# Kernel tuning notes

Hardware: AMD Instinct MI355X
Metric: run time of the kernel (lower is better)

## Reference

```python
import jax, jax.numpy as jnp
import numpy as np

N = 131072          # number of items ranked in one soft_rank call
CAPACITY = 3.0      # self.capcity in the torch module


def _pav_kl(y, w):
    """KL isotonic regression (non-increasing fit) via Pool-Adjacent-Violators.
    Pooled block value = logsumexp(y_block) - logsumexp(w_block).
    Matches torchsort / fast-soft-sort isotonic_kl. Sequential O(N)."""
    n = y.shape[0]

    def push(i, st):
        ly, lw, val, start, ptr = st
        ly = ly.at[ptr].set(y[i])
        lw = lw.at[ptr].set(w[i])
        val = val.at[ptr].set(y[i] - w[i])
        start = start.at[ptr].set(i)
        ptr = ptr + 1

        def cond(s):
            _, _, v, _, p = s
            return (p >= 2) & (v[p - 2] <= v[p - 1])

        def merge(s):
            ly, lw, v, stt, p = s
            ny = jnp.logaddexp(ly[p - 2], ly[p - 1])
            nw = jnp.logaddexp(lw[p - 2], lw[p - 1])
            return (ly.at[p - 2].set(ny), lw.at[p - 2].set(nw),
                    v.at[p - 2].set(ny - nw), stt, p - 1)

        return jax.lax.while_loop(cond, merge, (ly, lw, val, start, ptr))

    z = jnp.zeros((n,), y.dtype)
    st0 = (z, z, z, jnp.full((n,), n, jnp.int32), jnp.int32(0))
    ly, lw, val, start, ptr = jax.lax.fori_loop(0, n, push, st0)
    # invalidate stale stack slots, then map each element to its block value
    start = jnp.where(jnp.arange(n) < ptr, start, n)
    blk = jnp.searchsorted(start, jnp.arange(n), side='right') - 1
    return val[blk]


@jax.custom_vjp
def isotonic_kl(y, w):
    return _pav_kl(y, w)


def _iso_fwd(y, w):
    sol = _pav_kl(y, w)
    return sol, (y, w, sol)


def _iso_bwd(res, g):
    y, w, sol = res
    n = y.shape[0]
    # blocks = maximal runs of constant solution (exact equality by construction)
    blk = jnp.cumsum(jnp.concatenate([jnp.array([True]), sol[1:] != sol[:-1]])) - 1
    gsum = jax.ops.segment_sum(g, blk, num_segments=n)

    def seg_softmax(v):
        m = jax.ops.segment_max(v, blk, num_segments=n)
        lse = jnp.log(jax.ops.segment_sum(jnp.exp(v - m[blk]), blk, num_segments=n)) + m
        return jnp.exp(v - lse[blk])

    return seg_softmax(y) * gsum[blk], -seg_softmax(w) * gsum[blk]


isotonic_kl.defvjp(_iso_fwd, _iso_bwd)


def soft_rank_kl(scores):
    """torchsort.soft_rank(scores[None], regularization='kl'), strength=1, ascending."""
    n = scores.shape[0]
    w_log = jnp.log(jnp.arange(n, 0, -1, dtype=scores.dtype))  # log([n, ..., 1])
    perm = jnp.argsort(-scores)          # descending, stable
    s = scores[perm]
    sol = isotonic_kl(s, w_log)
    inv = jnp.argsort(perm)
    return jnp.exp(s - sol)[inv]


def setup_inputs() -> dict:
    key = jax.random.key(0)
    k = jax.random.split(key, 5)
    x = jax.random.normal(k[0], (N, 1), jnp.float32)
    # torch Linear default init bounds: 1/sqrt(fan_in)
    w1 = jax.random.uniform(k[1], (1, 32), jnp.float32, -1.0, 1.0)
    b1 = jax.random.uniform(k[2], (32,), jnp.float32, -1.0, 1.0)
    lim2 = 1.0 / np.sqrt(32.0)
    w2 = jax.random.uniform(k[3], (32, 1), jnp.float32, -lim2, lim2)
    b2 = jax.random.uniform(k[4], (1,), jnp.float32, -lim2, lim2)
    return {"x": x, "w1": w1, "b1": b1, "w2": w2, "b2": b2}


def reference(x, w1, b1, w2, b2):
    h = jnp.maximum(x @ w1 + b1, 0.0)            # [N, 32]
    scores = (h @ w2 + b2).reshape(-1)           # [N]
    ranks = soft_rank_kl(scores)                 # [N]
    other = jax.lax.stop_gradient(ranks) % CAPACITY
    ranks = (ranks - other) / CAPACITY + 1.0
    return ranks.reshape(-1, 1)
```

## Files before the change

### kernel.cpp

```cpp
#include <hip/hip_runtime.h>
#include <stdint.h>

typedef unsigned int u32;
typedef unsigned long long u64;

#define N_ITEMS 131072
#define NB 131072
#define NSLICE 8
#define CHUNK 64
#define NCHUNKS 2048
#define SCAN_BLOCKS 512
#define FIXSCALE 268435456.0f
#define FIXMASK ((1ull << 46) - 1)


__device__ __forceinline__ float wsumf(int s, int e) {
  return 0.5f * (float)(e - s + 1) * (float)(2 * N_ITEMS - s - e);
}

__device__ __forceinline__ float key_to_score(u32 key) {
  u32 m = ~key;
  u32 u = (m & 0x80000000u) ? (m ^ 0x80000000u) : ~m;
  return __uint_as_float(u);
}

#define LOG2E 1.4426950408889634f
__device__ __forceinline__ float fexp(float x) { return exp2f(x * LOG2E); }

__device__ __forceinline__ u32 bucket_of(u32 key, u32 kmin, u32 kmax) {
  double scale = (double)NB / ((double)(kmax - kmin) + 1.0);
  u32 b = (u32)((double)(key - kmin) * scale);
  return b < NB ? b : (NB - 1);
}


__global__ void score_key_kernel(const float* __restrict__ x,
                                 const float* __restrict__ w1,
                                 const float* __restrict__ b1,
                                 const float* __restrict__ w2,
                                 const float* __restrict__ b2,
                                 u32* __restrict__ keyRaw,
                                 u32* __restrict__ pmin, u32* __restrict__ pmax,
                                 u64* __restrict__ hist8, u64* __restrict__ flags) {
  __shared__ u32 r0[256], r1[256];
  int t = threadIdx.x;
  int i = blockIdx.x * 256 + t;
#pragma unroll
  for (int k = 0; k < NSLICE; ++k) hist8[(size_t)k * NB + i] = 0ull;
  if (i < SCAN_BLOCKS) flags[i] = 0ull;
  float xv = x[i];
  float s = b2[0];
#pragma unroll
  for (int j = 0; j < 32; ++j) {
    float h = fmaf(xv, w1[j], b1[j]);
    h = fmaxf(h, 0.0f);
    s = fmaf(h, w2[j], s);
  }
  u32 u = __float_as_uint(s);
  u32 m = u ^ ((u & 0x80000000u) ? 0xFFFFFFFFu : 0x80000000u);
  u32 key = ~m;
  keyRaw[i] = key;
  r0[t] = key; r1[t] = key;
  __syncthreads();
  for (int off = 128; off > 0; off >>= 1) {
    if (t < off) { r0[t] = min(r0[t], r0[t + off]); r1[t] = max(r1[t], r1[t + off]); }
    __syncthreads();
  }
  if (t == 0) { pmin[blockIdx.x] = r0[0]; pmax[blockIdx.x] = r1[0]; }
}


__global__ void hist_kernel(const u32* __restrict__ keyRaw,
                            const u32* __restrict__ pmin, const u32* __restrict__ pmax,
                            u64* __restrict__ hist8, u32* __restrict__ mm) {
  __shared__ u32 s0[256], s1[256];
  int t = threadIdx.x;
  s0[t] = min(pmin[t], pmin[t + 256]);
  s1[t] = max(pmax[t], pmax[t + 256]);
  __syncthreads();
  for (int off = 128; off > 0; off >>= 1) {
    if (t < off) { s0[t] = min(s0[t], s0[t + off]); s1[t] = max(s1[t], s1[t + off]); }
    __syncthreads();
  }
  u32 kmin = s0[0], kmax = s1[0];
  if (blockIdx.x == 0 && t == 0) { mm[0] = kmin; mm[1] = kmax; }
  int i = blockIdx.x * 256 + t;
  u32 key = keyRaw[i];
  u32 g = bucket_of(key, kmin, kmax);
  float smax = key_to_score(kmin);
  float v = fexp(key_to_score(key) - smax);
  u64 fix = (u64)fmaxf(1.0f, fmaf(v, FIXSCALE, 0.5f));
  size_t slice = (size_t)(blockIdx.x & (NSLICE - 1)) * NB;
  atomicAdd(&hist8[slice + g], (1ull << 46) | fix);
}


__global__ __launch_bounds__(256) void scan_pav_kernel(const u64* __restrict__ hist8,
                                                       u64* __restrict__ flags,
                                                       u32* __restrict__ cdf,
                                                       u32* __restrict__ cstart,
                                                       float* __restrict__ SY,
                                                       int* __restrict__ ST,
                                                       int* __restrict__ cnt) {
  __shared__ u32 sh[256];
  __shared__ float seL[256];
  __shared__ u32 cdfL[257];
  __shared__ u32 exclu_s;
  __shared__ u32 stkST[64][4];
  __shared__ float stkSY[64][4];
  int t = threadIdx.x, b = blockIdx.x;
  int i = b * 256 + t;
  u64 acc = 0;
#pragma unroll
  for (int c = 0; c < NSLICE; ++c) acc += hist8[(size_t)c * NB + i];
  u32 v = (u32)(acc >> 46);
  seL[t] = (float)(acc & FIXMASK) * (1.0f / FIXSCALE);
  sh[t] = v;
  __syncthreads();
  for (int off = 1; off < 256; off <<= 1) {
    u32 x2 = (t >= off) ? sh[t - off] : 0u;
    __syncthreads();
    sh[t] += x2;
    __syncthreads();
  }
  if (t == 0) {
    u32 agg = sh[255];
    if (b == 0) {
      atomicExch(&flags[0], (2ull << 32) | (u64)agg);
      exclu_s = 0u;
    } else {
      atomicExch(&flags[b], (1ull << 32) | (u64)agg);
      u32 ex = 0; int j = b - 1;
      for (;;) {
        u64 f = atomicAdd(&flags[j], 0ull);
        u32 st = (u32)(f >> 32);
        if (st == 0u) continue;
        ex += (u32)f;
        if (st == 2u) break;
        --j;
      }
      atomicExch(&flags[b], (2ull << 32) | (u64)(ex + agg));
      exclu_s = ex;
    }
  }
  __syncthreads();
  u32 exclu = exclu_s;
  u32 e = sh[t] - v + exclu;
  cdfL[t] = e;
  if (t == 255) cdfL[256] = exclu + sh[255];
  cdf[i] = e;
  if ((t & 63) == 0) cstart[i >> 6] = e;
  if (i == 0) cstart[NCHUNKS] = N_ITEMS;
  __syncthreads();
  if (t < 4) {
    int c = b * 4 + t;
    int ptr = 0; bool have = false;
    float syT = 0.0f; int stT = 0;
    for (int k = 0; k < 64; ++k) {
      u32 cs = cdfL[t * 64 + k], ce = cdfL[t * 64 + k + 1];
      if (ce == cs) continue;
      float syC = seL[t * 64 + k];
      int stC = (int)cs, eC = (int)ce - 1;
      while (have) {
        float SWc = wsumf(stC, eC);
        float SWt = wsumf(stT, stC - 1);
        if (!(syT * SWc <= syC * SWt)) break;
        syC += syT; stC = stT;
        if (ptr == 0) { have = false; break; }
        --ptr;
        stT = (int)stkST[ptr][t]; syT = stkSY[ptr][t];
      }
      if (have) { stkST[ptr][t] = (u32)stT; stkSY[ptr][t] = syT; ++ptr; }
      stT = stC; syT = syC; have = true;
    }
    int slotBase = c * 64;
    for (int k2 = 0; k2 < ptr; ++k2) {
      ST[slotBase + k2] = (int)stkST[k2][t];
      SY[slotBase + k2] = stkSY[k2][t];
    }
    int n = ptr;
    if (have) { ST[slotBase + n] = stT; SY[slotBase + n] = syT; ++n; }
    cnt[c] = n;
  }
}


__global__ void merge_multi_kernel(float* __restrict__ SY, int* __restrict__ ST,
                                   int* __restrict__ cnt, const u32* __restrict__ cstart,
                                   int l0, int L) {
  __shared__ int lcnt[64];
  __shared__ int ca[32], cb[32], cM[32];
  int t = threadIdx.x;
  int G = 1 << L;
  int SC = 1 << l0;
  int baseC = blockIdx.x * G * SC;
  if (t < G) lcnt[t] = cnt[baseC + t * SC];
  __syncthreads();
  for (int j = 0; j < L; ++j) {
    int P = G >> (j + 1);
    if (t < P) {
      int p = t;
      int kL = p << (j + 1), kR = kL + (1 << j);
      int slotL = (baseC + kL * SC) * 64, slotR = (baseC + kR * SC) * 64;
      int nL = lcnt[kL], nR = lcnt[kR];
      int a = 0, b = 0, hasM = 0;
      if (nL > 0 && nR > 0) {
        int gstartR = (int)cstart[baseC + kR * SC];
        int gendR   = (int)cstart[baseC + (kR + (1 << j)) * SC];
        float SYL = SY[slotL + nL - 1]; int stL = ST[slotL + nL - 1];
        float SYR = SY[slotR];
        int eR = (nR > 1) ? (ST[slotR + 1] - 1) : (gendR - 1);
        float SWL = wsumf(stL, gstartR - 1);
        float SWR = wsumf(gstartR, eR);
        if (SYL * SWR <= SYR * SWL) {
          hasM = 1;
          float SYM = SYL + SYR; int Ms = stL, Me = eR;
          a = 1; b = 1;
          for (;;) {
            float SWM = wsumf(Ms, Me);
            if (a < nL) {
              float SYe = SY[slotL + nL - 1 - a]; int ste = ST[slotL + nL - 1 - a];
              float SWe = wsumf(ste, Ms - 1);
              if (SYe * SWM <= SYM * SWe) { SYM += SYe; Ms = ste; ++a; continue; }
            }
            if (b < nR) {
              float SYb = SY[slotR + b]; int sb = ST[slotR + b];
              int eb = (b + 1 < nR) ? (ST[slotR + b + 1] - 1) : (gendR - 1);
              float SWb = wsumf(sb, eb);
              if (SYM * SWb <= SYb * SWM) { SYM += SYb; Me = eb; ++b; continue; }
            }
            break;
          }
          SY[slotL + nL - a] = SYM; ST[slotL + nL - a] = Ms;
        }
      }
      ca[p] = a; cb[p] = b; cM[p] = hasM;
    }
    __syncthreads();
    for (int p = 0; p < P; ++p) {
      int kL = p << (j + 1), kR = kL + (1 << j);
      int nL = lcnt[kL], nR = lcnt[kR];
      int a = ca[p], b = cb[p], hasM = cM[p];
      int slotL = (baseC + kL * SC) * 64, slotR = (baseC + kR * SC) * 64;
      int destBase = slotL + nL - a + hasM;
      int srcBase = slotR + b;
      int ncopy = nR - b;
      for (int off = 0; off < ncopy; off += blockDim.x) {
        int k2 = off + t; bool act = k2 < ncopy;
        float vs = 0.f; int vt = 0;
        if (act) { vs = SY[srcBase + k2]; vt = ST[srcBase + k2]; }
        __syncthreads();
        if (act) { SY[destBase + k2] = vs; ST[destBase + k2] = vt; }
        __syncthreads();
      }
    }
    __syncthreads();
    if (t < P) {
      int p = t; int kL = p << (j + 1), kR = kL + (1 << j);
      lcnt[kL] = lcnt[kL] - ca[p] + cM[p] + (lcnt[kR] - cb[p]);
    }
    __syncthreads();
  }
  if (t == 0) cnt[baseC] = lcnt[0];
}


__global__ void out_kernel(const u32* __restrict__ keyRaw, const u32* __restrict__ mm,
                           const u32* __restrict__ cdf,
                           const float* __restrict__ SY, const int* __restrict__ ST,
                           const int* __restrict__ cnt, float* __restrict__ out) {
  int i = blockIdx.x * 256 + threadIdx.x;
  u32 key = keyRaw[i];
  u32 kmin = mm[0], kmax = mm[1];
  float smax = key_to_score(kmin);
  u32 g = bucket_of(key, kmin, kmax);
  int p = (int)cdf[g];
  int m = cnt[0];
  int lo = 0, hi = m - 1;
  while (lo < hi) {
    int mid = (lo + hi + 1) >> 1;
    if (ST[mid] <= p) lo = mid; else hi = mid - 1;
  }
  int s0 = ST[lo];
  int e0 = (lo + 1 < m) ? (ST[lo + 1] - 1) : (N_ITEMS - 1);
  float SW = wsumf(s0, e0);
  float s = key_to_score(key);
  float rank = fexp(s - smax) * SW / SY[lo];
  out[i] = floorf(rank * (1.0f / 3.0f)) + 1.0f;
}


extern "C" void kernel_launch(void* const* d_in, const int* in_sizes, int n_in,
                              void* d_out, int out_size, void* d_ws, size_t ws_size,
                              hipStream_t stream) {
  const float* x  = (const float*)d_in[0];
  const float* w1 = (const float*)d_in[1];
  const float* b1 = (const float*)d_in[2];
  const float* w2 = (const float*)d_in[3];
  const float* b2 = (const float*)d_in[4];
  float* out = (float*)d_out;

  char* ws = (char*)d_ws;
  size_t o = 0;
  u32* mm     = (u32*)(ws + o); o += 16;
  u32* pmin   = (u32*)(ws + o); o += (size_t)SCAN_BLOCKS * 4;
  u32* pmax   = (u32*)(ws + o); o += (size_t)SCAN_BLOCKS * 4;
  u64* hist8  = (u64*)(ws + o); o += (size_t)NSLICE * NB * 8;
  u64* flags  = (u64*)(ws + o); o += (size_t)SCAN_BLOCKS * 8;
  u32* cdf    = (u32*)(ws + o); o += (size_t)(NB + 4) * 4;
  u32* cstart = (u32*)(ws + o); o += (size_t)(NCHUNKS + 4) * 4;
  u32* keyRaw = (u32*)(ws + o); o += (size_t)N_ITEMS * 4;
  float* SY   = (float*)(ws + o); o += (size_t)N_ITEMS * 4;
  int* ST     = (int*)(ws + o);   o += (size_t)N_ITEMS * 4;
  int* cnt    = (int*)(ws + o);   o += (size_t)NCHUNKS * 4;

  score_key_kernel<<<SCAN_BLOCKS, 256, 0, stream>>>(x, w1, b1, w2, b2,
                                                    keyRaw, pmin, pmax, hist8, flags);
  hist_kernel<<<SCAN_BLOCKS, 256, 0, stream>>>(keyRaw, pmin, pmax, hist8, mm);
  scan_pav_kernel<<<SCAN_BLOCKS, 256, 0, stream>>>(hist8, flags, cdf, cstart, SY, ST, cnt);
  merge_multi_kernel<<<64, 256, 0, stream>>>(SY, ST, cnt, cstart, 0, 5);
  merge_multi_kernel<<<1, 256, 0, stream>>>(SY, ST, cnt, cstart, 5, 6);
  out_kernel<<<SCAN_BLOCKS, 256, 0, stream>>>(keyRaw, mm, cdf, SY, ST, cnt, out);
}
```

Baseline: 134.4 us.

## Replace copy-based PAV block merging with in-place per-chunk deques plus compaction

Each chunk's PAV stack becomes a deque with packed begin/end indices and linked head/tail chunk pointers. Merging two neighbouring segments now pops from the deques in place instead of shifting the right stack's entries with block-wide copies and barriers. A prefix sum over the live entry counts and a new gather kernel compact the surviving blocks for the output binary search. This removes the serialized per-pair copy loops, at the cost of an extra kernel launch, chunk-scanning peek and pop logic, and more workspace.

```diff
diff --git a/kernel.cpp b/kernel.cpp
--- a/kernel.cpp
+++ b/kernel.cpp
@@ -31,6 +31,39 @@
   double scale = (double)NB / ((double)(kmax - kmin) + 1.0);
   u32 b = (u32)((double)(key - kmin) * scale);
   return b < NB ? b : (NB - 1);
+}
+
+
+__device__ __forceinline__ bool peek_next(const u32* be, int c1, int c, int k,
+                                          int& nc, int& nk) {
+  u32 w = be[c];
+  if (k + 1 < (int)(w & 0xFFFFu)) { nc = c; nk = k + 1; return true; }
+  for (int cc = c + 1; cc < c1; ++cc) {
+    w = be[cc];
+    if ((int)(w >> 16) < (int)(w & 0xFFFFu)) { nc = cc; nk = (int)(w >> 16); return true; }
+  }
+  return false;
+}
+
+__device__ __forceinline__ bool pop_tail(u32* be, int c0, int& tc, int& tk) {
+  be[tc] = (be[tc] & 0xFFFF0000u) | (u32)tk;
+  if ((int)(be[tc] >> 16) < tk) { --tk; return true; }
+  for (int c = tc - 1; c >= c0; --c) {
+    u32 w = be[c];
+    if ((int)(w >> 16) < (int)(w & 0xFFFFu)) { tc = c; tk = (int)(w & 0xFFFFu) - 1; return true; }
+  }
+  return false;
+}
+
+__device__ __forceinline__ bool pop_head(u32* be, int c1, int& hc, int& hk) {
+  be[hc] = (be[hc] & 0x0000FFFFu) | ((u32)(hk + 1) << 16);
+  u32 w = be[hc];
+  if ((int)(w >> 16) < (int)(w & 0xFFFFu)) { ++hk; return true; }
+  for (int c = hc + 1; c < c1; ++c) {
+    w = be[c];
+    if ((int)(w >> 16) < (int)(w & 0xFFFFu)) { hc = c; hk = (int)(w >> 16); return true; }
+  }
+  return false;
 }
 
 
@@ -101,7 +134,9 @@
                                                        u32* __restrict__ cstart,
                                                        float* __restrict__ SY,
                                                        int* __restrict__ ST,
-                                                       int* __restrict__ cnt) {
+                                                       u32* __restrict__ be,
+                                                       int* __restrict__ hC,
+                                                       int* __restrict__ tC) {
   __shared__ u32 sh[256];
   __shared__ float seL[256];
   __shared__ u32 cdfL[257];
@@ -180,112 +215,145 @@
     }
     int n = ptr;
     if (have) { ST[slotBase + n] = stT; SY[slotBase + n] = syT; ++n; }
-    cnt[c] = n;
-  }
-}
-
-
-__global__ void merge_multi_kernel(float* __restrict__ SY, int* __restrict__ ST,
-                                   int* __restrict__ cnt, const u32* __restrict__ cstart,
-                                   int l0, int L) {
-  __shared__ int lcnt[64];
-  __shared__ int ca[32], cb[32], cM[32];
+    be[c] = (u32)n;
+    hC[c] = tC[c] = (n > 0) ? c : -1;
+  }
+}
+
+
+__device__ void merge_pair(int c0, int cm, int c1,
+                           float* __restrict__ SY, int* __restrict__ ST,
+                           u32* __restrict__ be, int* __restrict__ hC, int* __restrict__ tC,
+                           const u32* __restrict__ cstart) {
+  int hR = hC[cm];
+  if (hR < 0) return;
+  int hL = hC[c0];
+  if (hL < 0) { hC[c0] = hR; tC[c0] = tC[cm]; return; }
+  int tL = tC[c0], tR = tC[cm];
+  int ltc = tL, ltk = (int)(be[tL] & 0xFFFFu) - 1;
+  float SYL = SY[ltc * 64 + ltk]; int stL = ST[ltc * 64 + ltk];
+  int eL = (int)cstart[cm] - 1;
+  int rhc = hR, rhk = (int)(be[hR] >> 16);
+  float SYR = SY[rhc * 64 + rhk]; int stR = ST[rhc * 64 + rhk];
+  int nc, nk;
+  int eR = peek_next(be, c1, rhc, rhk, nc, nk) ? ST[nc * 64 + nk] - 1
+                                               : (int)cstart[c1] - 1;
+  float SWL = wsumf(stL, eL);
+  float SWR = wsumf(stR, eR);
+  if (!(SYL * SWR <= SYR * SWL)) { tC[c0] = tR; return; }
+  float SYM = SYL + SYR; int Ms = stL, Me = eR;
+  int lastPc = ltc;
+  bool Lne = pop_tail(be, c0, ltc, ltk);
+  bool Rne = pop_head(be, c1, rhc, rhk);
+  for (;;) {
+    float SWM = wsumf(Ms, Me);
+    if (Lne) {
+      float SYe = SY[ltc * 64 + ltk]; int ste = ST[ltc * 64 + ltk];
+      float SWe = wsumf(ste, Ms - 1);
+      if (SYe * SWM <= SYM * SWe) {
+        SYM += SYe; Ms = ste;
+        lastPc = ltc;
+        Lne = pop_tail(be, c0, ltc, ltk);
+        continue;
+      }
+    }
+    if (Rne) {
+      float SYb = SY[rhc * 64 + rhk]; int sb = ST[rhc * 64 + rhk];
+      int eb = peek_next(be, c1, rhc, rhk, nc, nk) ? ST[nc * 64 + nk] - 1
+                                                   : (int)cstart[c1] - 1;
+      float SWb = wsumf(sb, eb);
+      if (SYM * SWb <= SYb * SWM) {
+        SYM += SYb; Me = eb;
+        Rne = pop_head(be, c1, rhc, rhk);
+        continue;
+      }
+    }
+    break;
+  }
+  u32 w = be[lastPc];
+  int ee = (int)(w & 0xFFFFu);
+  ST[lastPc * 64 + ee] = Ms; SY[lastPc * 64 + ee] = SYM;
+  be[lastPc] = (w & 0xFFFF0000u) | (u32)(ee + 1);
+  u32 hb = be[hL];
+  hC[c0] = ((int)(hb >> 16) < (int)(hb & 0xFFFFu)) ? hL : lastPc;
+  tC[c0] = Rne ? tR : lastPc;
+}
+
+__global__ void merge_deque_kernel(float* __restrict__ SY, int* __restrict__ ST,
+                                   u32* __restrict__ be, int* __restrict__ hC,
+                                   int* __restrict__ tC, const u32* __restrict__ cstart,
+                                   u32* __restrict__ pref,
+                                   int l0, int L, int do_pref) {
   int t = threadIdx.x;
   int G = 1 << L;
   int SC = 1 << l0;
   int baseC = blockIdx.x * G * SC;
-  if (t < G) lcnt[t] = cnt[baseC + t * SC];
-  __syncthreads();
   for (int j = 0; j < L; ++j) {
     int P = G >> (j + 1);
     if (t < P) {
-      int p = t;
-      int kL = p << (j + 1), kR = kL + (1 << j);
-      int slotL = (baseC + kL * SC) * 64, slotR = (baseC + kR * SC) * 64;
-      int nL = lcnt[kL], nR = lcnt[kR];
-      int a = 0, b = 0, hasM = 0;
-      if (nL > 0 && nR > 0) {
-        int gstartR = (int)cstart[baseC + kR * SC];
-        int gendR   = (int)cstart[baseC + (kR + (1 << j)) * SC];
-        float SYL = SY[slotL + nL - 1]; int stL = ST[slotL + nL - 1];
-        float SYR = SY[slotR];
-        int eR = (nR > 1) ? (ST[slotR + 1] - 1) : (gendR - 1);
-        float SWL = wsumf(stL, gstartR - 1);
-        float SWR = wsumf(gstartR, eR);
-        if (SYL * SWR <= SYR * SWL) {
-          hasM = 1;
-          float SYM = SYL + SYR; int Ms = stL, Me = eR;
-          a = 1; b = 1;
-          for (;;) {
-            float SWM = wsumf(Ms, Me);
-            if (a < nL) {
-              float SYe = SY[slotL + nL - 1 - a]; int ste = ST[slotL + nL - 1 - a];
-              float SWe = wsumf(ste, Ms - 1);
-              if (SYe * SWM <= SYM * SWe) { SYM += SYe; Ms = ste; ++a; continue; }
-            }
-            if (b < nR) {
-              float SYb = SY[slotR + b]; int sb = ST[slotR + b];
-              int eb = (b + 1 < nR) ? (ST[slotR + b + 1] - 1) : (gendR - 1);
-              float SWb = wsumf(sb, eb);
-              if (SYM * SWb <= SYb * SWM) { SYM += SYb; Me = eb; ++b; continue; }
-            }
-            break;
-          }
-          SY[slotL + nL - a] = SYM; ST[slotL + nL - a] = Ms;
-        }
-      }
-      ca[p] = a; cb[p] = b; cM[p] = hasM;
-    }
-    __syncthreads();
-    for (int p = 0; p < P; ++p) {
-      int kL = p << (j + 1), kR = kL + (1 << j);
-      int nL = lcnt[kL], nR = lcnt[kR];
-      int a = ca[p], b = cb[p], hasM = cM[p];
-      int slotL = (baseC + kL * SC) * 64, slotR = (baseC + kR * SC) * 64;
-      int destBase = slotL + nL - a + hasM;
-      int srcBase = slotR + b;
-      int ncopy = nR - b;
-      for (int off = 0; off < ncopy; off += blockDim.x) {
-        int k2 = off + t; bool act = k2 < ncopy;
-        float vs = 0.f; int vt = 0;
-        if (act) { vs = SY[srcBase + k2]; vt = ST[srcBase + k2]; }
-        __syncthreads();
-        if (act) { SY[destBase + k2] = vs; ST[destBase + k2] = vt; }
-        __syncthreads();
-      }
-    }
-    __syncthreads();
-    if (t < P) {
-      int p = t; int kL = p << (j + 1), kR = kL + (1 << j);
-      lcnt[kL] = lcnt[kL] - ca[p] + cM[p] + (lcnt[kR] - cb[p]);
-    }
-    __syncthreads();
-  }
-  if (t == 0) cnt[baseC] = lcnt[0];
+      int GC = SC << j;
+      int c0 = baseC + (t << (j + 1)) * SC;
+      merge_pair(c0, c0 + GC, c0 + 2 * GC, SY, ST, be, hC, tC, cstart);
+    }
+    __syncthreads();
+  }
+  if (do_pref) {
+    __shared__ u32 psum[256];
+    u32 loc[8]; u32 s = 0;
+    for (int q = 0; q < 8; ++q) {
+      u32 w = be[t * 8 + q];
+      loc[q] = s; s += (w & 0xFFFFu) - (w >> 16);
+    }
+    psum[t] = s;
+    __syncthreads();
+    for (int off = 1; off < 256; off <<= 1) {
+      u32 x2 = (t >= off) ? psum[t - off] : 0u;
+      __syncthreads();
+      psum[t] += x2;
+      __syncthreads();
+    }
+    u32 base = (t == 0) ? 0u : psum[t - 1];
+    for (int q = 0; q < 8; ++q) pref[t * 8 + q] = base + loc[q];
+    if (t == 255) pref[NCHUNKS] = psum[255];
+  }
+}
+
+
+__global__ void gather_kernel(const float* __restrict__ SY, const int* __restrict__ ST,
+                              const u32* __restrict__ be, const u32* __restrict__ pref,
+                              float* __restrict__ SYc, int* __restrict__ STc) {
+  int i = blockIdx.x * 256 + threadIdx.x;
+  int c = i >> 6, k = i & 63;
+  u32 w = be[c];
+  int b = (int)(w >> 16), e = (int)(w & 0xFFFFu);
+  if (k >= b && k < e) {
+    int dst = (int)pref[c] + (k - b);
+    STc[dst] = ST[i]; SYc[dst] = SY[i];
+  }
 }
 
 
 __global__ void out_kernel(const u32* __restrict__ keyRaw, const u32* __restrict__ mm,
-                           const u32* __restrict__ cdf,
-                           const float* __restrict__ SY, const int* __restrict__ ST,
-                           const int* __restrict__ cnt, float* __restrict__ out) {
+                           const u32* __restrict__ cdf, const u32* __restrict__ pref,
+                           const float* __restrict__ SYc, const int* __restrict__ STc,
+                           float* __restrict__ out) {
   int i = blockIdx.x * 256 + threadIdx.x;
   u32 key = keyRaw[i];
   u32 kmin = mm[0], kmax = mm[1];
   float smax = key_to_score(kmin);
   u32 g = bucket_of(key, kmin, kmax);
   int p = (int)cdf[g];
-  int m = cnt[0];
+  int m = (int)pref[NCHUNKS];
   int lo = 0, hi = m - 1;
   while (lo < hi) {
     int mid = (lo + hi + 1) >> 1;
-    if (ST[mid] <= p) lo = mid; else hi = mid - 1;
-  }
-  int s0 = ST[lo];
-  int e0 = (lo + 1 < m) ? (ST[lo + 1] - 1) : (N_ITEMS - 1);
+    if (STc[mid] <= p) lo = mid; else hi = mid - 1;
+  }
+  int s0 = STc[lo];
+  int e0 = (lo + 1 < m) ? (STc[lo + 1] - 1) : (N_ITEMS - 1);
   float SW = wsumf(s0, e0);
   float s = key_to_score(key);
-  float rank = fexp(s - smax) * SW / SY[lo];
+  float rank = fexp(s - smax) * SW / SYc[lo];
   out[i] = floorf(rank * (1.0f / 3.0f)) + 1.0f;
 }
 
@@ -309,16 +377,23 @@
   u64* flags  = (u64*)(ws + o); o += (size_t)SCAN_BLOCKS * 8;
   u32* cdf    = (u32*)(ws + o); o += (size_t)(NB + 4) * 4;
   u32* cstart = (u32*)(ws + o); o += (size_t)(NCHUNKS + 4) * 4;
+  u32* pref   = (u32*)(ws + o); o += (size_t)(NCHUNKS + 4) * 4;
   u32* keyRaw = (u32*)(ws + o); o += (size_t)N_ITEMS * 4;
   float* SY   = (float*)(ws + o); o += (size_t)N_ITEMS * 4;
   int* ST     = (int*)(ws + o);   o += (size_t)N_ITEMS * 4;
-  int* cnt    = (int*)(ws + o);   o += (size_t)NCHUNKS * 4;
+  float* SYc  = (float*)(ws + o); o += (size_t)N_ITEMS * 4;
+  int* STc    = (int*)(ws + o);   o += (size_t)N_ITEMS * 4;
+  u32* be     = (u32*)(ws + o);   o += (size_t)NCHUNKS * 4;
+  int* hC     = (int*)(ws + o);   o += (size_t)NCHUNKS * 4;
+  int* tC     = (int*)(ws + o);   o += (size_t)NCHUNKS * 4;
 
   score_key_kernel<<<SCAN_BLOCKS, 256, 0, stream>>>(x, w1, b1, w2, b2,
                                                     keyRaw, pmin, pmax, hist8, flags);
   hist_kernel<<<SCAN_BLOCKS, 256, 0, stream>>>(keyRaw, pmin, pmax, hist8, mm);
-  scan_pav_kernel<<<SCAN_BLOCKS, 256, 0, stream>>>(hist8, flags, cdf, cstart, SY, ST, cnt);
-  merge_multi_kernel<<<64, 256, 0, stream>>>(SY, ST, cnt, cstart, 0, 5);
-  merge_multi_kernel<<<1, 256, 0, stream>>>(SY, ST, cnt, cstart, 5, 6);
-  out_kernel<<<SCAN_BLOCKS, 256, 0, stream>>>(keyRaw, mm, cdf, SY, ST, cnt, out);
-}
+  scan_pav_kernel<<<SCAN_BLOCKS, 256, 0, stream>>>(hist8, flags, cdf, cstart,
+                                                   SY, ST, be, hC, tC);
+  merge_deque_kernel<<<64, 64, 0, stream>>>(SY, ST, be, hC, tC, cstart, pref, 0, 5, 0);
+  merge_deque_kernel<<<1, 256, 0, stream>>>(SY, ST, be, hC, tC, cstart, pref, 5, 6, 1);
+  gather_kernel<<<SCAN_BLOCKS, 256, 0, stream>>>(SY, ST, be, pref, SYc, STc);
+  out_kernel<<<SCAN_BLOCKS, 256, 0, stream>>>(keyRaw, mm, cdf, pref, SYc, STc, out);
+}
```

After: 193.5 us. 44.0% more time.

## Pack PAV block records into int2 and split final merge into two levels

Applied to the files above, without the earlier changes.

Stores each block's start index and log-sum value as one interleaved int2 record, so each merge and lookup step does one 8-byte load instead of two separate loads from different arrays. Halves the number of histogram slices, which cuts zeroing and reduction traffic but raises atomic contention per slice. Splits the final single-block 64-way merge into an 8-block 8-way stage followed by a 1024-thread 8-way stage, so more of the tree merge runs in parallel. The new last stage is launched with 1024 threads while the kernel's shared arrays are sized for a group count of at most 64.

```diff
diff --git a/kernel.cpp b/kernel.cpp
--- a/kernel.cpp
+++ b/kernel.cpp
@@ -6,7 +6,7 @@
 
 #define N_ITEMS 131072
 #define NB 131072
-#define NSLICE 8
+#define NSLICE 4
 #define CHUNK 64
 #define NCHUNKS 2048
 #define SCAN_BLOCKS 512
@@ -32,6 +32,8 @@
   u32 b = (u32)((double)(key - kmin) * scale);
   return b < NB ? b : (NB - 1);
 }
+
+__device__ __forceinline__ float recSY(int2 r) { return __int_as_float(r.y); }
 
 
 __global__ void score_key_kernel(const float* __restrict__ x,
@@ -99,8 +101,7 @@
                                                        u64* __restrict__ flags,
                                                        u32* __restrict__ cdf,
                                                        u32* __restrict__ cstart,
-                                                       float* __restrict__ SY,
-                                                       int* __restrict__ ST,
+                                                       int2* __restrict__ REC,
                                                        int* __restrict__ cnt) {
   __shared__ u32 sh[256];
   __shared__ float seL[256];
@@ -174,18 +175,16 @@
       stT = stC; syT = syC; have = true;
     }
     int slotBase = c * 64;
-    for (int k2 = 0; k2 < ptr; ++k2) {
-      ST[slotBase + k2] = (int)stkST[k2][t];
-      SY[slotBase + k2] = stkSY[k2][t];
-    }
+    for (int k2 = 0; k2 < ptr; ++k2)
+      REC[slotBase + k2] = make_int2((int)stkST[k2][t], __float_as_int(stkSY[k2][t]));
     int n = ptr;
-    if (have) { ST[slotBase + n] = stT; SY[slotBase + n] = syT; ++n; }
+    if (have) { REC[slotBase + n] = make_int2(stT, __float_as_int(syT)); ++n; }
     cnt[c] = n;
   }
 }
 
 
-__global__ void merge_multi_kernel(float* __restrict__ SY, int* __restrict__ ST,
+__global__ void merge_multi_kernel(int2* __restrict__ REC,
                                    int* __restrict__ cnt, const u32* __restrict__ cstart,
                                    int l0, int L) {
   __shared__ int lcnt[64];
@@ -207,9 +206,11 @@
       if (nL > 0 && nR > 0) {
         int gstartR = (int)cstart[baseC + kR * SC];
         int gendR   = (int)cstart[baseC + (kR + (1 << j)) * SC];
-        float SYL = SY[slotL + nL - 1]; int stL = ST[slotL + nL - 1];
-        float SYR = SY[slotR];
-        int eR = (nR > 1) ? (ST[slotR + 1] - 1) : (gendR - 1);
+        int2 rL = REC[slotL + nL - 1];
+        float SYL = recSY(rL); int stL = rL.x;
+        int2 rR = REC[slotR];
+        float SYR = recSY(rR);
+        int eR = (nR > 1) ? (REC[slotR + 1].x - 1) : (gendR - 1);
         float SWL = wsumf(stL, gstartR - 1);
         float SWR = wsumf(gstartR, eR);
         if (SYL * SWR <= SYR * SWL) {
@@ -219,19 +220,21 @@
           for (;;) {
             float SWM = wsumf(Ms, Me);
             if (a < nL) {
-              float SYe = SY[slotL + nL - 1 - a]; int ste = ST[slotL + nL - 1 - a];
+              int2 re = REC[slotL + nL - 1 - a];
+              float SYe = recSY(re); int ste = re.x;
               float SWe = wsumf(ste, Ms - 1);
               if (SYe * SWM <= SYM * SWe) { SYM += SYe; Ms = ste; ++a; continue; }
             }
             if (b < nR) {
-              float SYb = SY[slotR + b]; int sb = ST[slotR + b];
-              int eb = (b + 1 < nR) ? (ST[slotR + b + 1] - 1) : (gendR - 1);
+              int2 rb = REC[slotR + b];
+              float SYb = recSY(rb); int sb = rb.x;
+              int eb = (b + 1 < nR) ? (REC[slotR + b + 1].x - 1) : (gendR - 1);
               float SWb = wsumf(sb, eb);
               if (SYM * SWb <= SYb * SWM) { SYM += SYb; Me = eb; ++b; continue; }
             }
             break;
           }
-          SY[slotL + nL - a] = SYM; ST[slotL + nL - a] = Ms;
+          REC[slotL + nL - a] = make_int2(Ms, __float_as_int(SYM));
         }
       }
       ca[p] = a; cb[p] = b; cM[p] = hasM;
@@ -247,10 +250,10 @@
       int ncopy = nR - b;
       for (int off = 0; off < ncopy; off += blockDim.x) {
         int k2 = off + t; bool act = k2 < ncopy;
-        float vs = 0.f; int vt = 0;
-        if (act) { vs = SY[srcBase + k2]; vt = ST[srcBase + k2]; }
+        int2 vr = make_int2(0, 0);
+        if (act) vr = REC[srcBase + k2];
         __syncthreads();
-        if (act) { SY[destBase + k2] = vs; ST[destBase + k2] = vt; }
+        if (act) REC[destBase + k2] = vr;
         __syncthreads();
       }
     }
@@ -267,7 +270,7 @@
 
 __global__ void out_kernel(const u32* __restrict__ keyRaw, const u32* __restrict__ mm,
                            const u32* __restrict__ cdf,
-                           const float* __restrict__ SY, const int* __restrict__ ST,
+                           const int2* __restrict__ REC,
                            const int* __restrict__ cnt, float* __restrict__ out) {
   int i = blockIdx.x * 256 + threadIdx.x;
   u32 key = keyRaw[i];
@@ -279,13 +282,14 @@
   int lo = 0, hi = m - 1;
   while (lo < hi) {
     int mid = (lo + hi + 1) >> 1;
-    if (ST[mid] <= p) lo = mid; else hi = mid - 1;
-  }
-  int s0 = ST[lo];
-  int e0 = (lo + 1 < m) ? (ST[lo + 1] - 1) : (N_ITEMS - 1);
+    if (REC[mid].x <= p) lo = mid; else hi = mid - 1;
+  }
+  int2 r = REC[lo];
+  int s0 = r.x;
+  int e0 = (lo + 1 < m) ? (REC[lo + 1].x - 1) : (N_ITEMS - 1);
   float SW = wsumf(s0, e0);
   float s = key_to_score(key);
-  float rank = fexp(s - smax) * SW / SY[lo];
+  float rank = fexp(s - smax) * SW / recSY(r);
   out[i] = floorf(rank * (1.0f / 3.0f)) + 1.0f;
 }
 
@@ -310,15 +314,15 @@
   u32* cdf    = (u32*)(ws + o); o += (size_t)(NB + 4) * 4;
   u32* cstart = (u32*)(ws + o); o += (size_t)(NCHUNKS + 4) * 4;
   u32* keyRaw = (u32*)(ws + o); o += (size_t)N_ITEMS * 4;
-  float* SY   = (float*)(ws + o); o += (size_t)N_ITEMS * 4;
-  int* ST     = (int*)(ws + o);   o += (size_t)N_ITEMS * 4;
-  int* cnt    = (int*)(ws + o);   o += (size_t)NCHUNKS * 4;
+  int2* REC   = (int2*)(ws + o); o += (size_t)N_ITEMS * 8;
+  int* cnt    = (int*)(ws + o);  o += (size_t)NCHUNKS * 4;
 
   score_key_kernel<<<SCAN_BLOCKS, 256, 0, stream>>>(x, w1, b1, w2, b2,
                                                     keyRaw, pmin, pmax, hist8, flags);
   hist_kernel<<<SCAN_BLOCKS, 256, 0, stream>>>(keyRaw, pmin, pmax, hist8, mm);
-  scan_pav_kernel<<<SCAN_BLOCKS, 256, 0, stream>>>(hist8, flags, cdf, cstart, SY, ST, cnt);
-  merge_multi_kernel<<<64, 256, 0, stream>>>(SY, ST, cnt, cstart, 0, 5);
-  merge_multi_kernel<<<1, 256, 0, stream>>>(SY, ST, cnt, cstart, 5, 6);
-  out_kernel<<<SCAN_BLOCKS, 256, 0, stream>>>(keyRaw, mm, cdf, SY, ST, cnt, out);
-}
+  scan_pav_kernel<<<SCAN_BLOCKS, 256, 0, stream>>>(hist8, flags, cdf, cstart, REC, cnt);
+  merge_multi_kernel<<<64, 256, 0, stream>>>(REC, cnt, cstart, 0, 5);
+  merge_multi_kernel<<<8, 256, 0, stream>>>(REC, cnt, cstart, 5, 3);
+  merge_multi_kernel<<<1, 1024, 0, stream>>>(REC, cnt, cstart, 8, 3);
+  out_kernel<<<SCAN_BLOCKS, 256, 0, stream>>>(keyRaw, mm, cdf, REC, cnt, out);
+}
```

Result: no change. 133.2 us (-0.9%).
